# Optimization experiments

Measured on AMD Instinct MI355X. Metric: run time of the kernel, lower is better.

## Reference

```python
import jax, jax.numpy as jnp
import numpy as np

B, D, C_IN = 2, 64, 4
N1, N2, N3, N4 = 32, 64, 96, 128
MQ, K = 1024, 5
DN = ('NCDHW', 'OIDHW', 'NCDHW')
PAD = [(2, 2)] * 3  # centered 5^3 kernel, matches Minkowski offsets in [-2, 2]


def setup_inputs() -> dict:
    rng = np.random.default_rng(0)
    mask = rng.random((B, D, D, D)) < 0.2
    x_feat = (rng.standard_normal((B, C_IN, D, D, D)) * mask[:, None]).astype(np.float32)
    Q_F = rng.random((B, MQ, 2)).astype(np.float32)  # per-point quality features (2 channels)

    def conv(cin, cout):
        w = (rng.standard_normal((cout, cin, K, K, K)) / np.sqrt(cin * K ** 3)).astype(np.float32)
        b = (0.01 * rng.standard_normal(cout)).astype(np.float32)
        return w, b

    def gdn(c):
        beta = np.ones(c, np.float32)
        gamma = (1e-4 * rng.random((c, c, K, K, K))).astype(np.float32)
        gamma[np.arange(c), np.arange(c), K // 2, K // 2, K // 2] += 0.1
        return beta, gamma

    w1, b1 = conv(C_IN, N1)
    w2, b2 = conv(N1, N2)
    w3, b3 = conv(N2, N3)
    w4, b4 = conv(N3, N4)
    beta1, gamma1 = gdn(N1)
    beta2, gamma2 = gdn(N2)
    beta3, gamma3 = gdn(N3)
    out = dict(x_feat=x_feat, mask=mask, Q_F=Q_F,
               w1=w1, b1=b1, w2=w2, b2=b2, w3=w3, b3=b3, w4=w4, b4=b4,
               beta1=beta1, gamma1=gamma1, beta2=beta2, gamma2=gamma2,
               beta3=beta3, gamma3=gamma3)
    return {k: jnp.asarray(v) for k, v in out.items()}


def _conv3d(x, w, b, stride):
    y = jax.lax.conv_general_dilated(x, w, (stride,) * 3, PAD, dimension_numbers=DN)
    return y + b[None, :, None, None, None]


def _pool_mask(m):
    # Minkowski stride-2 output coords = any occupied input in each 2x2x2 cell
    b, d = m.shape[0], m.shape[1]
    return m.reshape(b, d // 2, 2, d // 2, 2, d // 2, 2).max(axis=(2, 4, 6))


def _gdn(x, beta, gamma, scale, m):
    # conditional GDN: y = x / sqrt(beta + conv5(gamma, x^2)), scaled per batch by q[:,0]
    den = jax.lax.conv_general_dilated(x * x, gamma, (1, 1, 1), PAD, dimension_numbers=DN)
    y = x * jax.lax.rsqrt(beta[None, :, None, None, None] + den)
    return y * scale * m[:, None]


def reference(x_feat, mask, Q_F, w1, b1, w2, b2, w3, b3, w4, b4,
              beta1, gamma1, beta2, gamma2, beta3, gamma3):
    m0 = mask.astype(x_feat.dtype)
    q = jnp.mean(Q_F, axis=1)[None]                       # [1, B, 2]: per-batch mean of Q.F
    scale = q[0, :, 0][:, None, None, None, None]         # per-batch conditional scale

    c0 = m0.sum(axis=(1, 2, 3))                           # count_per_batch(x)
    m1 = _pool_mask(m0)
    x = _gdn(_conv3d(x_feat, w1, b1, 2) * m1[:, None], beta1, gamma1, scale, m1)
    c1 = m1.sum(axis=(1, 2, 3))
    m2 = _pool_mask(m1)
    x = _gdn(_conv3d(x, w2, b2, 2) * m2[:, None], beta2, gamma2, scale, m2)
    c2 = m2.sum(axis=(1, 2, 3))
    m3 = _pool_mask(m2)
    x = _gdn(_conv3d(x, w3, b3, 2) * m3[:, None], beta3, gamma3, scale, m3)
    x = _conv3d(x, w4, b4, 1) * m3[:, None]               # stride-1 conv keeps coords
    k = jnp.stack([c2, c1, c0]).astype(jnp.int32)         # k.reverse() in the original
    return x, q, k
```

## Files before the change

### kernel.cpp

```cpp
#include <hip/hip_runtime.h>
#include <math.h>

constexpr int Bn  = 2;
constexpr int CIN = 4;
constexpr int MQn = 1024;
constexpr int D0 = 64, D1 = 32, D2 = 16, D3 = 8;

constexpr int OUT_X = 0;
constexpr int OUT_Q = 131072;
constexpr int OUT_K = 131076;

constexpr size_t OFF_CNT   = 0;
constexpr size_t OFF_ZERO  = 8;
constexpr size_t OFF_D1    = 16;
constexpr size_t OFF_T2    = OFF_D1 + 2097152;
constexpr size_t OFF_D2    = OFF_T2 + 524288;
constexpr size_t OFF_T3    = OFF_D2 + 524288;
constexpr size_t OFF_D3    = OFF_T3 + 98304;
constexpr size_t ZERO_END  = OFF_D3 + 98304;
constexpr size_t OFF_SCALE = 3342360;
constexpr size_t OFF_M1    = 3342368;
constexpr size_t OFF_M2    = OFF_M1 + 65536;
constexpr size_t OFF_M3    = OFF_M2 + 8192;
constexpr size_t OFF_T1    = OFF_M3 + 1024;
constexpr size_t OFF_Y1    = OFF_T1 + 2097152;
constexpr size_t OFF_Y2    = OFF_Y1 + 2097152;
constexpr size_t OFF_SQ1   = OFF_Y2 + 524288;
constexpr size_t OFF_SQ2   = OFF_SQ1 + 1048576;
constexpr size_t OFF_SQ3   = OFF_SQ2 + 262144;
constexpr size_t OFF_Y3C   = OFF_SQ3 + 49152;
constexpr size_t OFF_W1T   = OFF_Y3C + 49152;
constexpr size_t OFF_W2T   = OFF_W1T + 16000;
constexpr size_t OFF_W3T   = OFF_W2T + 256000;
constexpr size_t OFF_WB1   = OFF_W3T + 768000;
constexpr size_t OFF_WB2   = OFF_WB1 + 64000;
constexpr size_t OFF_WB3   = OFF_WB2 + 256000;
constexpr size_t OFF_WB4   = OFF_WB3 + 576000;
constexpr size_t OFF_P2    = 12248736;
constexpr size_t OFF_Y1HL  = OFF_P2 + 3145728;
constexpr size_t OFF_WB2S  = OFF_Y1HL + 3145728;
constexpr size_t OFF_WB1S  = OFF_WB2S + 384000;

typedef float v4f __attribute__((ext_vector_type(4)));
typedef __attribute__((ext_vector_type(8)))  short bf16x8v;
typedef __attribute__((ext_vector_type(4)))  short bf16x4v;
typedef __attribute__((ext_vector_type(16))) float f32x16v;

__device__ __forceinline__ void async_copy4(const float* g, float* l) {
    __builtin_amdgcn_global_load_lds(
        (const __attribute__((address_space(1))) void*)g,
        (__attribute__((address_space(3))) void*)l, 4, 0, 0);
}
__device__ __forceinline__ void async_copy16(const float* g, float* l) {
    __builtin_amdgcn_global_load_lds(
        (const __attribute__((address_space(1))) void*)g,
        (__attribute__((address_space(3))) void*)l, 16, 0, 0);
}
__device__ __forceinline__ unsigned short f2bf(float f) {
    unsigned u = __float_as_uint(f);
    return (unsigned short)((u + 0x7FFFu + ((u >> 16) & 1u)) >> 16);
}
__device__ __forceinline__ float bf2f(unsigned short h) {
    return __uint_as_float((unsigned)h << 16);
}

__global__ void qmean_kernel(const float* __restrict__ QF, float* __restrict__ out_q,
                             float* __restrict__ scale) {
    int b = blockIdx.x >> 1, c = blockIdx.x & 1;
    float s = 0.f;
    for (int m = threadIdx.x; m < MQn; m += blockDim.x)
        s += QF[(b * MQn + m) * 2 + c];
    __shared__ float sh[256];
    sh[threadIdx.x] = s;
    __syncthreads();
    for (int st = 128; st > 0; st >>= 1) {
        if (threadIdx.x < st) sh[threadIdx.x] += sh[threadIdx.x + st];
        __syncthreads();
    }
    if (threadIdx.x == 0) {
        float mean = sh[0] / (float)MQn;
        out_q[b * 2 + c] = mean;
        if (c == 0) scale[b] = mean;
    }
}

__global__ void mask_pool1_kernel(const float* __restrict__ xf, float* __restrict__ m1,
                                  float* __restrict__ c0) {
    int idx = blockIdx.x * blockDim.x + threadIdx.x;
    int b = idx >> 15;
    int v = idx & 32767;
    int oz = v >> 10, oy = (v >> 5) & 31, ox = v & 31;
    float cnt = 0.f, mx = 0.f;
    for (int dz = 0; dz < 2; ++dz)
        for (int dy = 0; dy < 2; ++dy)
            for (int dx = 0; dx < 2; ++dx) {
                int z = 2 * oz + dz, y = 2 * oy + dy, x = 2 * ox + dx;
                size_t base = (size_t)b * CIN * D0 * D0 * D0 + ((size_t)z * D0 + y) * D0 + x;
                bool occ = false;
                for (int c = 0; c < CIN; ++c)
                    occ = occ || (xf[base + (size_t)c * D0 * D0 * D0] != 0.f);
                if (occ) { cnt += 1.f; mx = 1.f; }
            }
    m1[idx] = mx;
    __shared__ float sh[256];
    sh[threadIdx.x] = cnt;
    __syncthreads();
    for (int st = 128; st > 0; st >>= 1) {
        if (threadIdx.x < st) sh[threadIdx.x] += sh[threadIdx.x + st];
        __syncthreads();
    }
    if (threadIdx.x == 0) atomicAdd(&c0[b], sh[0]);
}

__global__ void pool_kernel(const float* __restrict__ min_, float* __restrict__ mout,
                            float* __restrict__ cacc, int Din) {
    int Do = Din >> 1;
    int per = Do * Do * Do;
    int idx = blockIdx.x * blockDim.x + threadIdx.x;
    int b = idx / per;
    int v = idx % per;
    int oz = v / (Do * Do), oy = (v / Do) % Do, ox = v % Do;
    float s = 0.f, mx = 0.f;
    for (int dz = 0; dz < 2; ++dz)
        for (int dy = 0; dy < 2; ++dy)
            for (int dx = 0; dx < 2; ++dx) {
                float val = min_[(((size_t)b * Din + 2 * oz + dz) * Din + 2 * oy + dy) * Din + 2 * ox + dx];
                s += val;
                mx = fmaxf(mx, val);
            }
    mout[idx] = mx;
    __shared__ float sh[256];
    sh[threadIdx.x] = s;
    __syncthreads();
    for (int st = 128; st > 0; st >>= 1) {
        if (threadIdx.x < st) sh[threadIdx.x] += sh[threadIdx.x + st];
        __syncthreads();
    }
    if (threadIdx.x == 0) atomicAdd(&cacc[b], sh[0]);
}

__global__ void writek_kernel(const float* __restrict__ cnt, float* __restrict__ outk) {
    int i = threadIdx.x;
    if (i < 6) {
        int row = i >> 1, b = i & 1;
        float v = (row == 0) ? cnt[4 + b] : (row == 1 ? cnt[2 + b] : cnt[b]);
        outk[i] = v;
    }
}

constexpr int FS1 = 0,       FE1 = 16000;
constexpr int FS2 = 16000,   FE2 = 272000;
constexpr int FS3 = 272000,  FE3 = 1040000;
__global__ __launch_bounds__(256) void wtrans_all_kernel(
        const float* __restrict__ w1, const float* __restrict__ w2,
        const float* __restrict__ w3, float* __restrict__ ws) {
    int idx = blockIdx.x * 256 + threadIdx.x;
    if (idx >= FE3) return;
    const float* src; float* dst; int cin, local;
    if (idx < FE1)      { src = w1; dst = ws + OFF_W1T; cin = 4;  local = idx - FS1; }
    else if (idx < FE2) { src = w2; dst = ws + OFF_W2T; cin = 32; local = idx - FS2; }
    else                { src = w3; dst = ws + OFF_W3T; cin = 64; local = idx - FS3; }
    int per = cin * 125;
    int co = local / per;
    int r  = local % per;
    int ci = r / 125, tap = r % 125;
    int chunk = co >> 4, j = co & 15;
    dst[(((size_t)chunk * cin + ci) * 125 + tap) * 16 + j] = src[local];
}

constexpr int MS1 = 0,        ME1 = 128000;
constexpr int MS2 = 128000,   ME2 = 640000;
constexpr int MS3 = 640000,   ME3 = 1792000;
constexpr int MS4 = 1792000,  ME4 = 3328000;
__global__ __launch_bounds__(256) void mwtrans_all_kernel(
        const float* __restrict__ g1, const float* __restrict__ g2,
        const float* __restrict__ g3, const float* __restrict__ w4,
        float* __restrict__ ws) {
    int idx = blockIdx.x * 256 + threadIdx.x;
    if (idx >= ME4) return;
    const float* src; unsigned short* dst; int nchn, cin, o;
    if (idx < ME1)      { src = g1; dst = (unsigned short*)(ws + OFF_WB1); nchn = 1; cin = 32; o = idx - MS1; }
    else if (idx < ME2) { src = g2; dst = (unsigned short*)(ws + OFF_WB2); nchn = 2; cin = 64; o = idx - MS2; }
    else if (idx < ME3) { src = g3; dst = (unsigned short*)(ws + OFF_WB3); nchn = 3; cin = 96; o = idx - MS3; }
    else                { src = w4; dst = (unsigned short*)(ws + OFF_WB4); nchn = 4; cin = 96; o = idx - MS4; }
    int j  = o & 7;
    int kc = (o >> 3) & 1;
    int n  = (o >> 4) & 31;
    int q  = o >> 9;
    int tap = q % 125;
    int q2  = q / 125;
    int nch = q2 % nchn;
    int cs  = q2 / nchn;
    int co = nch * 32 + n;
    int ci = cs * 16 + kc * 8 + j;
    dst[o] = f2bf(src[((size_t)co * cin + ci) * 125 + tap]);
}

constexpr int W2S_N = 768000;
__global__ __launch_bounds__(256) void w2s_kernel(const float* __restrict__ w2,
        unsigned short* __restrict__ dst) {
    int o = blockIdx.x * 256 + threadIdx.x;
    if (o >= W2S_N) return;
    int j = o & 7; int kc = (o >> 3) & 1; int n = (o >> 4) & 31; int q = o >> 9;
    int tap = q % 125; int q2 = q / 125; int c = q2 & 1; int cs = q2 >> 1;
    int co = c * 32 + n;
    int e = cs * 16 + kc * 8 + j;
    int ci = e & 31;
    float wv = w2[((size_t)co * 32 + ci) * 125 + tap];
    unsigned short h = f2bf(wv);
    if (e >= 64) h = f2bf(wv - bf2f(h));
    dst[o] = h;
}

constexpr int W1S_N = 64000;
__global__ __launch_bounds__(256) void w1s_kernel(const float* __restrict__ w1,
        unsigned short* __restrict__ dst) {
    int o = blockIdx.x * 256 + threadIdx.x;
    if (o >= W1S_N) return;
    int j = o & 7; int kc = (o >> 3) & 1; int n = (o >> 4) & 31; int tap = o >> 9;
    int ci = j & 3;
    unsigned short h;
    float wv = w1[((size_t)n * 4 + ci) * 125 + tap];
    unsigned short hi = f2bf(wv);
    if (kc == 0)       h = hi;
    else if (j < 4)    h = f2bf(wv - bf2f(hi));
    else               h = 0;
    dst[o] = h;
}

__global__ __launch_bounds__(256) void xcl_kernel(const float* __restrict__ xf,
        unsigned short* __restrict__ xcl) {
    int idx = blockIdx.x * 256 + threadIdx.x;
    int s = idx & 262143; int b = idx >> 18;
    bf16x8v o;
#pragma unroll
    for (int ci = 0; ci < 4; ++ci) {
        float f = xf[((size_t)(b * 4 + ci) << 18) + s];
        unsigned short h = f2bf(f);
        o[ci] = (short)h;
        o[4 + ci] = (short)f2bf(f - bf2f(h));
    }
    *(bf16x8v*)(xcl + (size_t)idx * 8) = o;
}

__global__ __launch_bounds__(256) void mconv1_s2_kernel(
    const unsigned short* __restrict__ xcl,
    const unsigned short* __restrict__ wb,
    const float* __restrict__ bias, const float* __restrict__ mask,
    const float* __restrict__ zerow,
    float* __restrict__ t1, unsigned short* __restrict__ sqcl)
{
    constexpr int DIN = 64, DOUT = 32;
    constexpr int NTX = 4, NTY = 8;
    int r = blockIdx.x;
    int tx0 = (r % NTX) * 8; r /= NTX;
    int ty0 = (r % NTY) * 4; r /= NTY;
    int tz0 = (r % 8) * 4;   int b = r / 8;

    int tid = threadIdx.x;
    int lane = tid & 63, w = tid >> 6;
    int n = lane & 31, kc = lane >> 5;
    int oz = tz0 + w, oy = ty0 + (n >> 3), ox = tx0 + (n & 7);

    f32x16v acc;
#pragma unroll
    for (int i = 0; i < 16; ++i) acc[i] = 0.f;

#pragma unroll 1
    for (int kz = 0; kz < 5; ++kz) {
        int gz = 2 * oz + kz - 2;
        bool zok = (unsigned)gz < (unsigned)DIN;
#pragma unroll 1
        for (int ky = 0; ky < 5; ++ky) {
            int gy = 2 * oy + ky - 2;
            bool zyok = zok && ((unsigned)gy < (unsigned)DIN);
            long long rowbase = (((long long)(b * DIN + gz) * DIN + gy) * DIN) * 8;
#pragma unroll
            for (int kx = 0; kx < 5; ++kx) {
                int gx = 2 * ox + kx - 2;
                bool ok = zyok && ((unsigned)gx < (unsigned)DIN);
                const unsigned short* g = ok ? xcl + (rowbase + (long long)gx * 8)
                                             : (const unsigned short*)zerow;
                bf16x8v dfrag = *(const bf16x8v*)g;
                int tap = (kz * 5 + ky) * 5 + kx;
                const unsigned short* wp = wb + ((size_t)tap << 9) + n * 16 + kc * 8;
                bf16x8v wfrag = *(const bf16x8v*)wp;
                acc = __builtin_amdgcn_mfma_f32_32x32x16_bf16(wfrag, dfrag, acc, 0, 0, 0);
            }
        }
    }

    int sp = (oz * DOUT + oy) * DOUT + ox;
    float mval = mask[b * DOUT * DOUT * DOUT + sp];
#pragma unroll
    for (int q = 0; q < 4; ++q) {
        int co0 = 8 * q + 4 * kc;
        bf16x4v s4;
#pragma unroll
        for (int j = 0; j < 4; ++j) {
            int co = co0 + j;
            float v = (acc[4 * q + j] + bias[co]) * mval;
            t1[(size_t)(b * 32 + co) * 32768 + sp] = v;
            s4[j] = (short)f2bf(v * v);
        }
        *(bf16x4v*)(sqcl + ((size_t)(b * 32768 + sp)) * 32 + co0) = s4;
    }
}

template<int CINt, int COUTt, int DIN, int DOUT, int STRIDE, int CIG, bool SQW>
__global__ __launch_bounds__(256, 4) void conv_tile_kernel(
    const float* __restrict__ in, const float* __restrict__ wt,
    const float* __restrict__ bb, const float* __restrict__ mask,
    const float* __restrict__ zerow, float* __restrict__ out,
    unsigned short* __restrict__ sqcl)
{
    constexpr int TZO = 4, TY = 8, TX = 8;
    constexpr int LZ = (STRIDE == 1) ? TZO + 4 : 2 * TZO + 3;
    constexpr int LY = (STRIDE == 1) ? TY + 4 : 2 * TY + 3;
    constexpr int LX = (STRIDE == 1) ? TX + 4 : 2 * TX + 3;
    constexpr int LXP = (STRIDE == 2) ? (LX + 1) / 2 : 0;
    constexpr int ROWLEN = (STRIDE == 2) ? 2 * LXP : LX;
    constexpr int LN = LZ * LY * ROWLEN;
    constexpr int NLOAD = (LN + 255) / 256;
    constexpr int PADN = NLOAD * 256;
    constexpr int NTZ = DOUT / TZO, NTY = DOUT / TY, NTX = DOUT / TX;
    constexpr int NT = NTZ * NTY * NTX;
    constexpr int NCHk = COUTt / 16;
    constexpr int CIPER = CINt / CIG;
    __shared__ float sh[2][PADN];
    __shared__ float wbuf[2][2048];

    int tile  = blockIdx.x % NT;
    int chunk = (blockIdx.x / NT) % NCHk;
    int cig   = (blockIdx.x / (NT * NCHk)) % CIG;
    int b     = blockIdx.x / (NT * NCHk * CIG);
    int tz0 = (tile / (NTY * NTX)) * TZO;
    int ty0 = ((tile / NTX) % NTY) * TY;
    int tx0 = (tile % NTX) * TX;
    int co0 = chunk * 16;

    int tid = threadIdx.x;
    int tx = tid & (TX - 1);
    int ty = (tid >> 3) & (TY - 1);
    int tz = tid >> 6;

    int iz0 = tz0 * STRIDE - 2, iy0 = ty0 * STRIDE - 2, ix0 = tx0 * STRIDE - 2;

    int goff[NLOAD];
#pragma unroll
    for (int k = 0; k < NLOAD; ++k) {
        int i = tid + k * 256;
        int c = i % ROWLEN; int rem = i / ROWLEN;
        int ly = rem % LY, lz = rem / LY;
        int lx;
        if (STRIDE == 2) { int p = c / LXP, xp = c % LXP; lx = 2 * xp + p; }
        else lx = c;
        int gz = iz0 + lz, gy = iy0 + ly, gx = ix0 + lx;
        bool valid = (i < LN) && (lx < LX) &&
                     (unsigned)gz < (unsigned)DIN && (unsigned)gy < (unsigned)DIN &&
                     (unsigned)gx < (unsigned)DIN;
        goff[k] = valid ? ((gz * DIN + gy) * DIN + gx) : -1;
    }

    int ci0 = cig * CIPER;
    auto stage = [&](int ci, int buf) {
        const float* base = in + (size_t)(b * CINt + ci) * DIN * DIN * DIN;
        float* dst = &sh[buf][0];
#pragma unroll
        for (int k = 0; k < NLOAD; ++k) {
            const float* g = (goff[k] >= 0) ? (base + goff[k]) : zerow;
            async_copy4(g, &dst[k * 256 + tid]);
        }
        const float* wsrc = wt + (size_t)(chunk * CINt + ci) * 2000;
#pragma unroll
        for (int k = 0; k < 2; ++k) {
            int f0 = (k * 256 + tid) * 4;
            const float* g = (f0 < 2000) ? (wsrc + f0) : zerow;
            async_copy16(g, &wbuf[buf][f0]);
        }
    };

    float acc[16];
#pragma unroll
    for (int j = 0; j < 16; ++j) acc[j] = 0.f;

    stage(ci0, 0);
#pragma unroll 1
    for (int i = 0; i < CIPER; ++i) {
        int cur = i & 1;
        __syncthreads();
        if (i + 1 < CIPER) stage(ci0 + i + 1, cur ^ 1);
        const float* shc = &sh[cur][0];
        const float* wb = &wbuf[cur][0];
#pragma unroll 1
        for (int kz = 0; kz < 5; ++kz) {
#pragma unroll 1
            for (int ky = 0; ky < 5; ++ky) {
                const float* rp = shc + ((tz * STRIDE + kz) * LY + ty * STRIDE + ky) * ROWLEN + tx;
                const float* wrow = wb + (kz * 5 + ky) * 5 * 16;
#pragma unroll
                for (int kx = 0; kx < 5; ++kx) {
                    float d = (STRIDE == 2) ? rp[(kx & 1) * LXP + (kx >> 1)] : rp[kx];
#pragma unroll
                    for (int q = 0; q < 4; ++q) {
                        v4f w = *(const v4f*)&wrow[kx * 16 + q * 4];
                        acc[4 * q + 0] = fmaf(d, w.x, acc[4 * q + 0]);
                        acc[4 * q + 1] = fmaf(d, w.y, acc[4 * q + 1]);
                        acc[4 * q + 2] = fmaf(d, w.z, acc[4 * q + 2]);
                        acc[4 * q + 3] = fmaf(d, w.w, acc[4 * q + 3]);
                    }
                }
            }
        }
    }

    int z = tz0 + tz, y = ty0 + ty, x = tx0 + tx;
    size_t sp = ((size_t)z * DOUT + y) * DOUT + x;
    if (CIG > 1) {
#pragma unroll
        for (int j = 0; j < 16; ++j) {
            size_t oidx = (size_t)(b * COUTt + co0 + j) * DOUT * DOUT * DOUT + sp;
            atomicAdd(&out[oidx], acc[j]);
        }
    } else {
        float mval = mask[(size_t)b * DOUT * DOUT * DOUT + sp];
        float vals[16];
#pragma unroll
        for (int j = 0; j < 16; ++j) {
            int co = co0 + j;
            size_t oidx = (size_t)(b * COUTt + co) * DOUT * DOUT * DOUT + sp;
            vals[j] = (acc[j] + bb[co]) * mval;
            out[oidx] = vals[j];
        }
        if (SQW) {
            bf16x8v s0, s1;
#pragma unroll
            for (int j = 0; j < 8; ++j) {
                s0[j] = (short)f2bf(vals[j] * vals[j]);
                s1[j] = (short)f2bf(vals[j + 8] * vals[j + 8]);
            }
            size_t cl = ((size_t)b * DOUT * DOUT * DOUT + sp) * COUTt + co0;
            *(bf16x8v*)(sqcl + cl) = s0;
            *(bf16x8v*)(sqcl + cl + 8) = s1;
        }
    }
}

__global__ __launch_bounds__(128) void gdn_cl1_kernel(const float* __restrict__ t,
        const float* __restrict__ den, const float* __restrict__ beta,
        const float* __restrict__ scale, unsigned short* __restrict__ yhl) {
    int idx = blockIdx.x * 128 + threadIdx.x;
    int sp = idx & 32767; int b = idx >> 15;
    float sc = scale[b];
    bf16x8v blk[12];
#pragma unroll
    for (int g = 0; g < 4; ++g) {
#pragma unroll
        for (int j = 0; j < 8; ++j) {
            int ci = g * 8 + j;
            size_t p = (size_t)(b * 32 + ci) * 32768 + sp;
            float v = t[p] * rsqrtf(beta[ci] + den[p]) * sc;
            unsigned short h = f2bf(v);
            blk[g][j] = (short)h;
            blk[4 + g][j] = (short)f2bf(v - bf2f(h));
            blk[8 + g][j] = (short)h;
        }
    }
    unsigned short* o = yhl + (size_t)idx * 96;
#pragma unroll
    for (int g = 0; g < 12; ++g) *(bf16x8v*)(o + g * 8) = blk[g];
}

template<int CINe, int COUTt, int DIN, int DOUT>
__global__ __launch_bounds__(256) void mconv_s2_kernel(
    const unsigned short* __restrict__ in,
    const unsigned short* __restrict__ wb,
    const float* __restrict__ zerow,
    float* __restrict__ pout)
{
    constexpr int NCH = COUTt / 32;
    constexpr int NTZ = DOUT / 4, NTY = DOUT / 4, NTX = DOUT / 8;
    constexpr int NT = NTZ * NTY * NTX * Bn;
    constexpr int VOX = DOUT * DOUT * DOUT;

    int tile = blockIdx.x % NT; int cs = blockIdx.x / NT;
    int r = tile;
    int tx0 = (r % NTX) * 8; r /= NTX;
    int ty0 = (r % NTY) * 4; r /= NTY;
    int tz0 = (r % NTZ) * 4; int b = r / NTZ;

    int tid = threadIdx.x;
    int lane = tid & 63, w = tid >> 6;
    int n = lane & 31, kc = lane >> 5;
    int oz = tz0 + w, oy = ty0 + (n >> 3), ox = tx0 + (n & 7);

    f32x16v acc[NCH];
#pragma unroll
    for (int c = 0; c < NCH; ++c)
#pragma unroll
        for (int i = 0; i < 16; ++i) acc[c][i] = 0.f;

#pragma unroll 1
    for (int kz = 0; kz < 5; ++kz) {
        int gz = 2 * oz + kz - 2;
        bool zok = (unsigned)gz < (unsigned)DIN;
#pragma unroll 1
        for (int ky = 0; ky < 5; ++ky) {
            int gy = 2 * oy + ky - 2;
            bool zyok = zok && ((unsigned)gy < (unsigned)DIN);
            long long rowbase = (((long long)(b * DIN + gz) * DIN + gy) * DIN) * CINe
                                + cs * 16 + kc * 8;
#pragma unroll
            for (int kx = 0; kx < 5; ++kx) {
                int gx = 2 * ox + kx - 2;
                bool ok = zyok && ((unsigned)gx < (unsigned)DIN);
                const unsigned short* g = ok ? in + (rowbase + (long long)gx * CINe)
                                             : (const unsigned short*)zerow;
                bf16x8v dfrag = *(const bf16x8v*)g;
                int tap = (kz * 5 + ky) * 5 + kx;
#pragma unroll
                for (int c = 0; c < NCH; ++c) {
                    const unsigned short* wp =
                        wb + (((size_t)(cs * NCH + c) * 125 + tap) << 9) + n * 16 + kc * 8;
                    bf16x8v wfrag = *(const bf16x8v*)wp;
                    acc[c] = __builtin_amdgcn_mfma_f32_32x32x16_bf16(wfrag, dfrag, acc[c], 0, 0, 0);
                }
            }
        }
    }

    int sp = (oz * DOUT + oy) * DOUT + ox;
#pragma unroll
    for (int c = 0; c < NCH; ++c) {
#pragma unroll
        for (int rr = 0; rr < 16; ++rr) {
            int co = c * 32 + (rr & 3) + 8 * (rr >> 2) + 4 * kc;
            pout[((size_t)(cs * Bn + b) * COUTt + co) * VOX + sp] = acc[c][rr];
        }
    }
}

__global__ __launch_bounds__(256) void red_epi2_kernel(const float* __restrict__ P,
        const float* __restrict__ bias, const float* __restrict__ mask,
        float* __restrict__ buf, unsigned short* __restrict__ sqcl) {
    constexpr int VOX = 4096;
    constexpr int NTOT = Bn * 64 * VOX;
    int idx = blockIdx.x * 256 + threadIdx.x;
    if (idx >= NTOT) return;
    int sp = idx % VOX;
    int co = (idx / VOX) & 63;
    int b = idx / (VOX * 64);
    float s = 0.f;
#pragma unroll
    for (int k = 0; k < 6; ++k) s += P[(size_t)k * NTOT + idx];
    float v = (s + bias[co]) * mask[b * VOX + sp];
    buf[idx] = v;
    sqcl[((size_t)b * VOX + sp) * 64 + co] = f2bf(v * v);
}

template<int CINt, int COUTt, int Dd, int TZ, int YB, int CIG, int ZSPL>
__global__ __launch_bounds__(256) void mconv_kernel(
    const unsigned short* __restrict__ in,
    const unsigned short* __restrict__ wb,
    const float* __restrict__ zerow,
    float* __restrict__ dout)
{
    constexpr int NCH = COUTt / 32;
    constexpr int LZ = TZ + 4, LYH = YB * 4 + 4, LXH = 12;
    constexpr int HV = LZ * LYH * LXH;
    constexpr int UN = 2 * HV;
    constexpr int NLOAD = (UN + 255) / 256;
    constexpr int NTZ = Dd / TZ, NTY = Dd / (YB * 4), NTX = Dd / 8;
    constexpr int NT = NTZ * NTY * NTX * Bn;
    __shared__ unsigned short lds[NLOAD * 256 * 8];

    int bid = blockIdx.x;
    int tile = bid % NT; int rest = bid / NT;
    int cs = rest % CIG; int zig = rest / CIG;
    int r = tile;
    int tx0 = (r % NTX) * 8; r /= NTX;
    int ty0 = (r % NTY) * (YB * 4); r /= NTY;
    int tz0 = (r % NTZ) * TZ; int b = r / NTZ;

    int tid = threadIdx.x;
    int iz0 = tz0 - 2, iy0 = ty0 - 2, ix0 = tx0 - 2;
#pragma unroll
    for (int k = 0; k < NLOAD; ++k) {
        int u = tid + k * 256;
        int v = u >> 1, half = u & 1;
        int lx = v % LXH; int t = v / LXH;
        int ly = t % LYH, lz = t / LYH;
        int gz = iz0 + lz, gy = iy0 + ly, gx = ix0 + lx;
        bool valid = (v < HV) &&
                     (unsigned)gz < (unsigned)Dd && (unsigned)gy < (unsigned)Dd &&
                     (unsigned)gx < (unsigned)Dd;
        const unsigned short* g = valid
            ? in + ((((size_t)b * Dd + gz) * Dd + gy) * Dd + gx) * CINt + cs * 16 + half * 8
            : (const unsigned short*)zerow;
        async_copy16((const float*)g, (float*)&lds[(size_t)u * 8]);
    }
    __syncthreads();

    int lane = tid & 63, w = tid >> 6;
    int zz = (YB == 1) ? w : (w >> 1);
    int yb = (YB == 1) ? 0 : (w & 1);
    int n = lane & 31, kc = lane >> 5;
    int vy = yb * 4 + (n >> 3), vx = n & 7;

    f32x16v acc[NCH];
#pragma unroll
    for (int c = 0; c < NCH; ++c)
#pragma unroll
        for (int i = 0; i < 16; ++i) acc[c][i] = 0.f;

    int kzlo = (ZSPL == 5) ? zig : 0;
    int kzhi = (ZSPL == 5) ? zig + 1 : 5;
#pragma unroll 1
    for (int kz = kzlo; kz < kzhi; ++kz) {
#pragma unroll 1
        for (int ky = 0; ky < 5; ++ky) {
            int hvrow = ((zz + kz) * LYH + (vy + ky)) * LXH + vx;
#pragma unroll
            for (int kx = 0; kx < 5; ++kx) {
                bf16x8v dfrag = *(const bf16x8v*)&lds[(size_t)(hvrow + kx) * 16 + kc * 8];
                int tap = (kz * 5 + ky) * 5 + kx;
#pragma unroll
                for (int c = 0; c < NCH; ++c) {
                    const unsigned short* wp =
                        wb + (((size_t)(cs * NCH + c) * 125 + tap) << 9) + n * 16 + kc * 8;
                    bf16x8v wfrag = *(const bf16x8v*)wp;
                    acc[c] = __builtin_amdgcn_mfma_f32_32x32x16_bf16(wfrag, dfrag, acc[c], 0, 0, 0);
                }
            }
        }
    }

    int sp = ((tz0 + zz) * Dd + (ty0 + vy)) * Dd + (tx0 + vx);
#pragma unroll
    for (int c = 0; c < NCH; ++c) {
#pragma unroll
        for (int rr = 0; rr < 16; ++rr) {
            int co = c * 32 + (rr & 3) + 8 * (rr >> 2) + 4 * kc;
            atomicAdd(&dout[(size_t)(b * COUTt + co) * Dd * Dd * Dd + sp], acc[c][rr]);
        }
    }
}

template<int COUTt, int DOUT, bool SQ>
__global__ __launch_bounds__(256) void conv_epi_kernel(float* __restrict__ buf,
        const float* __restrict__ bias, const float* __restrict__ mask,
        unsigned short* __restrict__ sqcl) {
    constexpr int VOX = DOUT * DOUT * DOUT;
    int idx = blockIdx.x * 256 + threadIdx.x;
    if (idx >= Bn * COUTt * VOX) return;
    int sp = idx % VOX;
    int co = (idx / VOX) % COUTt;
    int b = idx / (VOX * COUTt);
    float v = (buf[idx] + bias[co]) * mask[b * VOX + sp];
    buf[idx] = v;
    if (SQ) sqcl[((size_t)b * VOX + sp) * COUTt + co] = f2bf(v * v);
}

template<int COUTt, int DOUT, bool CL>
__global__ __launch_bounds__(256) void gdn_epi_kernel(const float* __restrict__ t,
        const float* __restrict__ den, const float* __restrict__ beta,
        const float* __restrict__ scale, float* __restrict__ y,
        unsigned short* __restrict__ ycl) {
    constexpr int VOX = DOUT * DOUT * DOUT;
    int idx = blockIdx.x * 256 + threadIdx.x;
    if (idx >= Bn * COUTt * VOX) return;
    int sp = idx % VOX;
    int co = (idx / VOX) % COUTt;
    int b = idx / (VOX * COUTt);
    float v = t[idx] * rsqrtf(beta[co] + den[idx]) * scale[b];
    if (CL) ycl[((size_t)b * VOX + sp) * COUTt + co] = f2bf(v);
    else    y[idx] = v;
}

extern "C" void kernel_launch(void* const* d_in, const int* in_sizes, int n_in,
                              void* d_out, int out_size, void* d_ws, size_t ws_size,
                              hipStream_t stream) {
    const float* x_feat = (const float*)d_in[0];
    const float* QF     = (const float*)d_in[2];
    const float* w1 = (const float*)d_in[3];  const float* b1 = (const float*)d_in[4];
    const float* w2 = (const float*)d_in[5];  const float* b2 = (const float*)d_in[6];
    const float* w3 = (const float*)d_in[7];  const float* b3 = (const float*)d_in[8];
    const float* w4 = (const float*)d_in[9];  const float* b4 = (const float*)d_in[10];
    const float* beta1 = (const float*)d_in[11]; const float* gamma1 = (const float*)d_in[12];
    const float* beta2 = (const float*)d_in[13]; const float* gamma2 = (const float*)d_in[14];
    const float* beta3 = (const float*)d_in[15]; const float* gamma3 = (const float*)d_in[16];

    float* out = (float*)d_out;
    float* ws = (float*)d_ws;
    float* cnt   = ws + OFF_CNT;
    float* zerow = ws + OFF_ZERO;
    float* scale = ws + OFF_SCALE;
    float* m1 = ws + OFF_M1;  float* m2 = ws + OFF_M2;  float* m3 = ws + OFF_M3;
    float* t1 = ws + OFF_T1;  float* d1 = ws + OFF_D1;
    float* t2 = ws + OFF_T2;  float* d2 = ws + OFF_D2;  float* y2 = ws + OFF_Y2;
    float* t3 = ws + OFF_T3;  float* d3 = ws + OFF_D3;
    float* p2 = ws + OFF_P2;
    unsigned short* sq1 = (unsigned short*)(ws + OFF_SQ1);
    unsigned short* sq2 = (unsigned short*)(ws + OFF_SQ2);
    unsigned short* sq3 = (unsigned short*)(ws + OFF_SQ3);
    unsigned short* y3c = (unsigned short*)(ws + OFF_Y3C);
    unsigned short* y1hl = (unsigned short*)(ws + OFF_Y1HL);
    unsigned short* xcl = (unsigned short*)(ws + OFF_Y1);
    float* w3T = ws + OFF_W3T;
    unsigned short* wb1 = (unsigned short*)(ws + OFF_WB1);
    unsigned short* wb2 = (unsigned short*)(ws + OFF_WB2);
    unsigned short* wb3 = (unsigned short*)(ws + OFF_WB3);
    unsigned short* wb4 = (unsigned short*)(ws + OFF_WB4);
    unsigned short* wb2s = (unsigned short*)(ws + OFF_WB2S);
    unsigned short* wb1s = (unsigned short*)(ws + OFF_WB1S);

    hipMemsetAsync(ws, 0, ZERO_END * sizeof(float), stream);
    hipMemsetAsync(out + OUT_X, 0, 131072 * sizeof(float), stream);

    qmean_kernel<<<4, 256, 0, stream>>>(QF, out + OUT_Q, scale);
    mask_pool1_kernel<<<256, 256, 0, stream>>>(x_feat, m1, cnt + 0);
    pool_kernel<<<32, 256, 0, stream>>>(m1, m2, cnt + 2, D1);
    pool_kernel<<<4, 256, 0, stream>>>(m2, m3, cnt + 4, D2);
    writek_kernel<<<1, 64, 0, stream>>>(cnt, out + OUT_K);

    wtrans_all_kernel<<<(FE3 + 255) / 256, 256, 0, stream>>>(w1, w2, w3, ws);
    mwtrans_all_kernel<<<(ME4 + 255) / 256, 256, 0, stream>>>(gamma1, gamma2, gamma3, w4, ws);
    w2s_kernel<<<(W2S_N + 255) / 256, 256, 0, stream>>>(w2, wb2s);
    w1s_kernel<<<(W1S_N + 255) / 256, 256, 0, stream>>>(w1, wb1s);
    xcl_kernel<<<2048, 256, 0, stream>>>(x_feat, xcl);

    mconv1_s2_kernel<<<512, 256, 0, stream>>>(xcl, wb1s, b1, m1, zerow, t1, sq1);
    mconv_kernel<32, 32, 32, 4, 1, 2, 1>
        <<<1024, 256, 0, stream>>>(sq1, wb1, zerow, d1);
    gdn_cl1_kernel<<<512, 128, 0, stream>>>(t1, d1, beta1, scale, y1hl);

    mconv_s2_kernel<96, 64, 32, 16>
        <<<64 * 6, 256, 0, stream>>>(y1hl, wb2s, zerow, p2);
    red_epi2_kernel<<<2048, 256, 0, stream>>>(p2, b2, m2, t2, sq2);
    mconv_kernel<64, 64, 16, 4, 1, 4, 1>
        <<<256, 256, 0, stream>>>(sq2, wb2, zerow, d2);
    gdn_epi_kernel<64, 16, false><<<2048, 256, 0, stream>>>(t2, d2, beta2, scale, y2, nullptr);

    conv_tile_kernel<64, 96, 16, 8, 2, 8, false>
        <<<192, 256, 0, stream>>>(y2, w3T, nullptr, nullptr, zerow, t3, nullptr);
    conv_epi_kernel<96, 8, true><<<384, 256, 0, stream>>>(t3, b3, m3, sq3);
    mconv_kernel<96, 96, 8, 2, 2, 6, 5>
        <<<240, 256, 0, stream>>>(sq3, wb3, zerow, d3);
    gdn_epi_kernel<96, 8, true><<<384, 256, 0, stream>>>(t3, d3, beta3, scale, nullptr, y3c);

    mconv_kernel<96, 128, 8, 2, 2, 6, 5>
        <<<240, 256, 0, stream>>>(y3c, wb4, zerow, out + OUT_X);
    conv_epi_kernel<128, 8, false><<<512, 256, 0, stream>>>(out + OUT_X, b4, m3, nullptr);
}
```

Before: 468.4 us.

## Move stage-3 strided conv from FP32 tile kernel to split-bf16 MFMA path

Replaces the FP32 scalar-FMA conv_tile_kernel for the third stride-2 convolution with the existing MFMA-based mconv_s2_kernel. Inputs are emitted in hi/lo bf16 channels-last form by a new GDN kernel, and weights are packed by a new w3s kernel, so the split-bf16 products keep near-FP32 accuracy. The work is split across channel slices into partial buffers, which a generalized reduce-epilogue kernel sums and then applies bias, mask and the squared output. The cost is extra workspace, one more weight-prep pass, and fewer blocks (96) for the conv.

```diff
diff --git a/kernel.cpp b/kernel.cpp
--- a/kernel.cpp
+++ b/kernel.cpp
@@ -40,17 +40,15 @@
 constexpr size_t OFF_Y1HL  = OFF_P2 + 3145728;
 constexpr size_t OFF_WB2S  = OFF_Y1HL + 3145728;
 constexpr size_t OFF_WB1S  = OFF_WB2S + 384000;
+constexpr size_t OFF_WB3S  = OFF_WB1S + 32000;
+constexpr size_t OFF_P3    = OFF_WB3S + 1152000;
+constexpr size_t OFF_Y2HL  = OFF_P3 + 1179648;
 
 typedef float v4f __attribute__((ext_vector_type(4)));
 typedef __attribute__((ext_vector_type(8)))  short bf16x8v;
 typedef __attribute__((ext_vector_type(4)))  short bf16x4v;
 typedef __attribute__((ext_vector_type(16))) float f32x16v;
 
-__device__ __forceinline__ void async_copy4(const float* g, float* l) {
-    __builtin_amdgcn_global_load_lds(
-        (const __attribute__((address_space(1))) void*)g,
-        (__attribute__((address_space(3))) void*)l, 4, 0, 0);
-}
 __device__ __forceinline__ void async_copy16(const float* g, float* l) {
     __builtin_amdgcn_global_load_lds(
         (const __attribute__((address_space(1))) void*)g,
@@ -146,26 +144,6 @@
         float v = (row == 0) ? cnt[4 + b] : (row == 1 ? cnt[2 + b] : cnt[b]);
         outk[i] = v;
     }
-}
-
-constexpr int FS1 = 0,       FE1 = 16000;
-constexpr int FS2 = 16000,   FE2 = 272000;
-constexpr int FS3 = 272000,  FE3 = 1040000;
-__global__ __launch_bounds__(256) void wtrans_all_kernel(
-        const float* __restrict__ w1, const float* __restrict__ w2,
-        const float* __restrict__ w3, float* __restrict__ ws) {
-    int idx = blockIdx.x * 256 + threadIdx.x;
-    if (idx >= FE3) return;
-    const float* src; float* dst; int cin, local;
-    if (idx < FE1)      { src = w1; dst = ws + OFF_W1T; cin = 4;  local = idx - FS1; }
-    else if (idx < FE2) { src = w2; dst = ws + OFF_W2T; cin = 32; local = idx - FS2; }
-    else                { src = w3; dst = ws + OFF_W3T; cin = 64; local = idx - FS3; }
-    int per = cin * 125;
-    int co = local / per;
-    int r  = local % per;
-    int ci = r / 125, tap = r % 125;
-    int chunk = co >> 4, j = co & 15;
-    dst[(((size_t)chunk * cin + ci) * 125 + tap) * 16 + j] = src[local];
 }
 
 constexpr int MS1 = 0,        ME1 = 128000;
@@ -212,6 +190,22 @@
     dst[o] = h;
 }
 
+constexpr int W3S_N = 2304000;
+__global__ __launch_bounds__(256) void w3s_kernel(const float* __restrict__ w3,
+        unsigned short* __restrict__ dst) {
+    int o = blockIdx.x * 256 + threadIdx.x;
+    if (o >= W3S_N) return;
+    int j = o & 7; int kc = (o >> 3) & 1; int n = (o >> 4) & 31; int q = o >> 9;
+    int tap = q % 125; int q2 = q / 125; int nch = q2 % 3; int cs = q2 / 3;
+    int co = nch * 32 + n;
+    int e = cs * 16 + kc * 8 + j;
+    int ci = e & 63;
+    float wv = w3[((size_t)co * 64 + ci) * 125 + tap];
+    unsigned short h = f2bf(wv);
+    if (e >= 128) h = f2bf(wv - bf2f(h));
+    dst[o] = h;
+}
+
 constexpr int W1S_N = 64000;
 __global__ __launch_bounds__(256) void w1s_kernel(const float* __restrict__ w1,
         unsigned short* __restrict__ dst) {
@@ -307,145 +301,6 @@
     }
 }
 
-template<int CINt, int COUTt, int DIN, int DOUT, int STRIDE, int CIG, bool SQW>
-__global__ __launch_bounds__(256, 4) void conv_tile_kernel(
-    const float* __restrict__ in, const float* __restrict__ wt,
-    const float* __restrict__ bb, const float* __restrict__ mask,
-    const float* __restrict__ zerow, float* __restrict__ out,
-    unsigned short* __restrict__ sqcl)
-{
-    constexpr int TZO = 4, TY = 8, TX = 8;
-    constexpr int LZ = (STRIDE == 1) ? TZO + 4 : 2 * TZO + 3;
-    constexpr int LY = (STRIDE == 1) ? TY + 4 : 2 * TY + 3;
-    constexpr int LX = (STRIDE == 1) ? TX + 4 : 2 * TX + 3;
-    constexpr int LXP = (STRIDE == 2) ? (LX + 1) / 2 : 0;
-    constexpr int ROWLEN = (STRIDE == 2) ? 2 * LXP : LX;
-    constexpr int LN = LZ * LY * ROWLEN;
-    constexpr int NLOAD = (LN + 255) / 256;
-    constexpr int PADN = NLOAD * 256;
-    constexpr int NTZ = DOUT / TZO, NTY = DOUT / TY, NTX = DOUT / TX;
-    constexpr int NT = NTZ * NTY * NTX;
-    constexpr int NCHk = COUTt / 16;
-    constexpr int CIPER = CINt / CIG;
-    __shared__ float sh[2][PADN];
-    __shared__ float wbuf[2][2048];
-
-    int tile  = blockIdx.x % NT;
-    int chunk = (blockIdx.x / NT) % NCHk;
-    int cig   = (blockIdx.x / (NT * NCHk)) % CIG;
-    int b     = blockIdx.x / (NT * NCHk * CIG);
-    int tz0 = (tile / (NTY * NTX)) * TZO;
-    int ty0 = ((tile / NTX) % NTY) * TY;
-    int tx0 = (tile % NTX) * TX;
-    int co0 = chunk * 16;
-
-    int tid = threadIdx.x;
-    int tx = tid & (TX - 1);
-    int ty = (tid >> 3) & (TY - 1);
-    int tz = tid >> 6;
-
-    int iz0 = tz0 * STRIDE - 2, iy0 = ty0 * STRIDE - 2, ix0 = tx0 * STRIDE - 2;
-
-    int goff[NLOAD];
-#pragma unroll
-    for (int k = 0; k < NLOAD; ++k) {
-        int i = tid + k * 256;
-        int c = i % ROWLEN; int rem = i / ROWLEN;
-        int ly = rem % LY, lz = rem / LY;
-        int lx;
-        if (STRIDE == 2) { int p = c / LXP, xp = c % LXP; lx = 2 * xp + p; }
-        else lx = c;
-        int gz = iz0 + lz, gy = iy0 + ly, gx = ix0 + lx;
-        bool valid = (i < LN) && (lx < LX) &&
-                     (unsigned)gz < (unsigned)DIN && (unsigned)gy < (unsigned)DIN &&
-                     (unsigned)gx < (unsigned)DIN;
-        goff[k] = valid ? ((gz * DIN + gy) * DIN + gx) : -1;
-    }
-
-    int ci0 = cig * CIPER;
-    auto stage = [&](int ci, int buf) {
-        const float* base = in + (size_t)(b * CINt + ci) * DIN * DIN * DIN;
-        float* dst = &sh[buf][0];
-#pragma unroll
-        for (int k = 0; k < NLOAD; ++k) {
-            const float* g = (goff[k] >= 0) ? (base + goff[k]) : zerow;
-            async_copy4(g, &dst[k * 256 + tid]);
-        }
-        const float* wsrc = wt + (size_t)(chunk * CINt + ci) * 2000;
-#pragma unroll
-        for (int k = 0; k < 2; ++k) {
-            int f0 = (k * 256 + tid) * 4;
-            const float* g = (f0 < 2000) ? (wsrc + f0) : zerow;
-            async_copy16(g, &wbuf[buf][f0]);
-        }
-    };
-
-    float acc[16];
-#pragma unroll
-    for (int j = 0; j < 16; ++j) acc[j] = 0.f;
-
-    stage(ci0, 0);
-#pragma unroll 1
-    for (int i = 0; i < CIPER; ++i) {
-        int cur = i & 1;
-        __syncthreads();
-        if (i + 1 < CIPER) stage(ci0 + i + 1, cur ^ 1);
-        const float* shc = &sh[cur][0];
-        const float* wb = &wbuf[cur][0];
-#pragma unroll 1
-        for (int kz = 0; kz < 5; ++kz) {
-#pragma unroll 1
-            for (int ky = 0; ky < 5; ++ky) {
-                const float* rp = shc + ((tz * STRIDE + kz) * LY + ty * STRIDE + ky) * ROWLEN + tx;
-                const float* wrow = wb + (kz * 5 + ky) * 5 * 16;
-#pragma unroll
-                for (int kx = 0; kx < 5; ++kx) {
-                    float d = (STRIDE == 2) ? rp[(kx & 1) * LXP + (kx >> 1)] : rp[kx];
-#pragma unroll
-                    for (int q = 0; q < 4; ++q) {
-                        v4f w = *(const v4f*)&wrow[kx * 16 + q * 4];
-                        acc[4 * q + 0] = fmaf(d, w.x, acc[4 * q + 0]);
-                        acc[4 * q + 1] = fmaf(d, w.y, acc[4 * q + 1]);
-                        acc[4 * q + 2] = fmaf(d, w.z, acc[4 * q + 2]);
-                        acc[4 * q + 3] = fmaf(d, w.w, acc[4 * q + 3]);
-                    }
-                }
-            }
-        }
-    }
-
-    int z = tz0 + tz, y = ty0 + ty, x = tx0 + tx;
-    size_t sp = ((size_t)z * DOUT + y) * DOUT + x;
-    if (CIG > 1) {
-#pragma unroll
-        for (int j = 0; j < 16; ++j) {
-            size_t oidx = (size_t)(b * COUTt + co0 + j) * DOUT * DOUT * DOUT + sp;
-            atomicAdd(&out[oidx], acc[j]);
-        }
-    } else {
-        float mval = mask[(size_t)b * DOUT * DOUT * DOUT + sp];
-        float vals[16];
-#pragma unroll
-        for (int j = 0; j < 16; ++j) {
-            int co = co0 + j;
-            size_t oidx = (size_t)(b * COUTt + co) * DOUT * DOUT * DOUT + sp;
-            vals[j] = (acc[j] + bb[co]) * mval;
-            out[oidx] = vals[j];
-        }
-        if (SQW) {
-            bf16x8v s0, s1;
-#pragma unroll
-            for (int j = 0; j < 8; ++j) {
-                s0[j] = (short)f2bf(vals[j] * vals[j]);
-                s1[j] = (short)f2bf(vals[j + 8] * vals[j + 8]);
-            }
-            size_t cl = ((size_t)b * DOUT * DOUT * DOUT + sp) * COUTt + co0;
-            *(bf16x8v*)(sqcl + cl) = s0;
-            *(bf16x8v*)(sqcl + cl + 8) = s1;
-        }
-    }
-}
-
 __global__ __launch_bounds__(128) void gdn_cl1_kernel(const float* __restrict__ t,
         const float* __restrict__ den, const float* __restrict__ beta,
         const float* __restrict__ scale, unsigned short* __restrict__ yhl) {
@@ -471,6 +326,32 @@
     for (int g = 0; g < 12; ++g) *(bf16x8v*)(o + g * 8) = blk[g];
 }
 
+__global__ __launch_bounds__(128) void gdn_cl2_kernel(const float* __restrict__ t,
+        const float* __restrict__ den, const float* __restrict__ beta,
+        const float* __restrict__ scale, unsigned short* __restrict__ yhl) {
+    int idx = blockIdx.x * 128 + threadIdx.x;
+    if (idx >= Bn * 4096) return;
+    int sp = idx & 4095; int b = idx >> 12;
+    float sc = scale[b];
+    bf16x8v blk[24];
+#pragma unroll
+    for (int g = 0; g < 8; ++g) {
+#pragma unroll
+        for (int j = 0; j < 8; ++j) {
+            int ci = g * 8 + j;
+            size_t p = (size_t)(b * 64 + ci) * 4096 + sp;
+            float v = t[p] * rsqrtf(beta[ci] + den[p]) * sc;
+            unsigned short h = f2bf(v);
+            blk[g][j] = (short)h;
+            blk[8 + g][j] = (short)f2bf(v - bf2f(h));
+            blk[16 + g][j] = (short)h;
+        }
+    }
+    unsigned short* o = yhl + (size_t)idx * 192;
+#pragma unroll
+    for (int g = 0; g < 24; ++g) *(bf16x8v*)(o + g * 8) = blk[g];
+}
+
 template<int CINe, int COUTt, int DIN, int DOUT>
 __global__ __launch_bounds__(256) void mconv_s2_kernel(
     const unsigned short* __restrict__ in,
@@ -479,7 +360,7 @@
     float* __restrict__ pout)
 {
     constexpr int NCH = COUTt / 32;
-    constexpr int NTZ = DOUT / 4, NTY = DOUT / 4, NTX = DOUT / 8;
+    constexpr int NTZ = DOUT / 4, NTY = DOUT / 4, NTX = (DOUT >= 8) ? DOUT / 8 : 1;
     constexpr int NT = NTZ * NTY * NTX * Bn;
     constexpr int VOX = DOUT * DOUT * DOUT;
 
@@ -540,22 +421,22 @@
     }
 }
 
-__global__ __launch_bounds__(256) void red_epi2_kernel(const float* __restrict__ P,
+template<int CS, int COUTt, int VOX>
+__global__ __launch_bounds__(256) void red_epi_kernel(const float* __restrict__ P,
         const float* __restrict__ bias, const float* __restrict__ mask,
         float* __restrict__ buf, unsigned short* __restrict__ sqcl) {
-    constexpr int VOX = 4096;
-    constexpr int NTOT = Bn * 64 * VOX;
+    constexpr int NTOT = Bn * COUTt * VOX;
     int idx = blockIdx.x * 256 + threadIdx.x;
     if (idx >= NTOT) return;
     int sp = idx % VOX;
-    int co = (idx / VOX) & 63;
-    int b = idx / (VOX * 64);
+    int co = (idx / VOX) % COUTt;
+    int b = idx / (VOX * COUTt);
     float s = 0.f;
 #pragma unroll
-    for (int k = 0; k < 6; ++k) s += P[(size_t)k * NTOT + idx];
+    for (int k = 0; k < CS; ++k) s += P[(size_t)k * NTOT + idx];
     float v = (s + bias[co]) * mask[b * VOX + sp];
     buf[idx] = v;
-    sqcl[((size_t)b * VOX + sp) * 64 + co] = f2bf(v * v);
+    sqcl[((size_t)b * VOX + sp) * COUTt + co] = f2bf(v * v);
 }
 
 template<int CINt, int COUTt, int Dd, int TZ, int YB, int CIG, int ZSPL>
@@ -697,22 +578,23 @@
     float* scale = ws + OFF_SCALE;
     float* m1 = ws + OFF_M1;  float* m2 = ws + OFF_M2;  float* m3 = ws + OFF_M3;
     float* t1 = ws + OFF_T1;  float* d1 = ws + OFF_D1;
-    float* t2 = ws + OFF_T2;  float* d2 = ws + OFF_D2;  float* y2 = ws + OFF_Y2;
+    float* t2 = ws + OFF_T2;  float* d2 = ws + OFF_D2;
     float* t3 = ws + OFF_T3;  float* d3 = ws + OFF_D3;
-    float* p2 = ws + OFF_P2;
+    float* p2 = ws + OFF_P2;  float* p3 = ws + OFF_P3;
     unsigned short* sq1 = (unsigned short*)(ws + OFF_SQ1);
     unsigned short* sq2 = (unsigned short*)(ws + OFF_SQ2);
     unsigned short* sq3 = (unsigned short*)(ws + OFF_SQ3);
     unsigned short* y3c = (unsigned short*)(ws + OFF_Y3C);
     unsigned short* y1hl = (unsigned short*)(ws + OFF_Y1HL);
+    unsigned short* y2hl = (unsigned short*)(ws + OFF_Y2HL);
     unsigned short* xcl = (unsigned short*)(ws + OFF_Y1);
-    float* w3T = ws + OFF_W3T;
     unsigned short* wb1 = (unsigned short*)(ws + OFF_WB1);
     unsigned short* wb2 = (unsigned short*)(ws + OFF_WB2);
     unsigned short* wb3 = (unsigned short*)(ws + OFF_WB3);
     unsigned short* wb4 = (unsigned short*)(ws + OFF_WB4);
+    unsigned short* wb1s = (unsigned short*)(ws + OFF_WB1S);
     unsigned short* wb2s = (unsigned short*)(ws + OFF_WB2S);
-    unsigned short* wb1s = (unsigned short*)(ws + OFF_WB1S);
+    unsigned short* wb3s = (unsigned short*)(ws + OFF_WB3S);
 
     hipMemsetAsync(ws, 0, ZERO_END * sizeof(float), stream);
     hipMemsetAsync(out + OUT_X, 0, 131072 * sizeof(float), stream);
@@ -723,10 +605,10 @@
     pool_kernel<<<4, 256, 0, stream>>>(m2, m3, cnt + 4, D2);
     writek_kernel<<<1, 64, 0, stream>>>(cnt, out + OUT_K);
 
-    wtrans_all_kernel<<<(FE3 + 255) / 256, 256, 0, stream>>>(w1, w2, w3, ws);
     mwtrans_all_kernel<<<(ME4 + 255) / 256, 256, 0, stream>>>(gamma1, gamma2, gamma3, w4, ws);
+    w1s_kernel<<<(W1S_N + 255) / 256, 256, 0, stream>>>(w1, wb1s);
     w2s_kernel<<<(W2S_N + 255) / 256, 256, 0, stream>>>(w2, wb2s);
-    w1s_kernel<<<(W1S_N + 255) / 256, 256, 0, stream>>>(w1, wb1s);
+    w3s_kernel<<<(W3S_N + 255) / 256, 256, 0, stream>>>(w3, wb3s);
     xcl_kernel<<<2048, 256, 0, stream>>>(x_feat, xcl);
 
     mconv1_s2_kernel<<<512, 256, 0, stream>>>(xcl, wb1s, b1, m1, zerow, t1, sq1);
@@ -736,14 +618,14 @@
 
     mconv_s2_kernel<96, 64, 32, 16>
         <<<64 * 6, 256, 0, stream>>>(y1hl, wb2s, zerow, p2);
-    red_epi2_kernel<<<2048, 256, 0, stream>>>(p2, b2, m2, t2, sq2);
+    red_epi_kernel<6, 64, 4096><<<2048, 256, 0, stream>>>(p2, b2, m2, t2, sq2);
     mconv_kernel<64, 64, 16, 4, 1, 4, 1>
         <<<256, 256, 0, stream>>>(sq2, wb2, zerow, d2);
-    gdn_epi_kernel<64, 16, false><<<2048, 256, 0, stream>>>(t2, d2, beta2, scale, y2, nullptr);
-
-    conv_tile_kernel<64, 96, 16, 8, 2, 8, false>
-        <<<192, 256, 0, stream>>>(y2, w3T, nullptr, nullptr, zerow, t3, nullptr);
-    conv_epi_kernel<96, 8, true><<<384, 256, 0, stream>>>(t3, b3, m3, sq3);
+    gdn_cl2_kernel<<<64, 128, 0, stream>>>(t2, d2, beta2, scale, y2hl);
+
+    mconv_s2_kernel<192, 96, 16, 8>
+        <<<8 * 12, 256, 0, stream>>>(y2hl, wb3s, zerow, p3);
+    red_epi_kernel<12, 96, 512><<<384, 256, 0, stream>>>(p3, b3, m3, t3, sq3);
     mconv_kernel<96, 96, 8, 2, 2, 6, 5>
         <<<240, 256, 0, stream>>>(sq3, wb3, zerow, d3);
     gdn_epi_kernel<96, 8, true><<<384, 256, 0, stream>>>(t3, d3, beta3, scale, nullptr, y3c);
```

Result: slower. 496.4 us (+6.0%).
